# Kernel tuning notes

Hardware: AMD Instinct MI355X
Metric: run time of the kernel (lower is better)

Reference implementation:

```python
import math
import jax, jax.numpy as jnp
import numpy as np

L, H, E, D = 12, 12, 768, 64   # stack_size, mh_size, embedding_dim, dim_w_matrices
B, S = 4, 512
EPS = 1e-5


def positional_enc(seq_len, model_dim):
    # faithful: power_ind = 10000 XOR int(2*i/dim)
    i = np.arange(model_dim)
    p = np.bitwise_xor(10000, (2 * i) // model_dim).astype(np.float32)
    pos = np.arange(seq_len, dtype=np.float32)[:, None]
    ang = pos / p[None, :]
    pe = np.where(i % 2 == 0, np.sin(ang), np.cos(ang)).astype(np.float32)
    return jnp.asarray(pe)


def layer_norm(x, g, b):
    mu = jnp.mean(x, axis=-1, keepdims=True)
    var = jnp.mean(jnp.square(x - mu), axis=-1, keepdims=True)
    return (x - mu) * jax.lax.rsqrt(var + EPS) * g + b


def encoder(x, wq, wo, g1, b1, fw, fb, g2, b2):
    # x: [B,S,E]; wq: [H,E,D]; wo: [E,H*D]; fw: [E,E] (torch Linear layout)
    bs = x.shape[0] * x.shape[1]
    nb = x.reshape(bs, E)                              # flatten batch (faithful)
    q = jnp.einsum('ne,hed->hnd', nb, wq)              # q == k == v (bug kept)
    scores = jax.nn.softmax(jnp.einsum('hnd,hmd->hnm', q, q) / math.sqrt(D), axis=-1)
    z = jnp.einsum('hnm,hmd->hnd', scores, q)          # [H,BS,D]
    zc = z.reshape(H * D, bs)                          # per-head view(D,-1) + cat
    mh = (wo @ zc).reshape(x.shape)                    # [B,S,E]
    l1 = layer_norm(x + mh, g1, b1)
    ffn = l1 @ fw.T + fb
    return layer_norm(l1 + ffn, g2, b2)


def setup_inputs() -> dict:
    key = jax.random.key(0)
    ks = jax.random.split(key, 8)

    def xavier(k, shape, fan_in, fan_out):
        lim = math.sqrt(6.0 / (fan_in + fan_out))
        return jax.random.uniform(k, shape, jnp.float32, -lim, lim)

    return {
        'tokens': jax.random.normal(ks[0], (B, S, E), jnp.float32),
        'wq':    xavier(ks[1], (L, H, E, D), E, D),
        'wo':    xavier(ks[2], (L, E, H * D), E, H * D),
        'ln1_g': jnp.ones((L, E), jnp.float32),
        'ln1_b': jnp.zeros((L, E), jnp.float32),
        'ffn_w': xavier(ks[3], (L, E, E), E, E),
        'ffn_b': jnp.zeros((L, E), jnp.float32),
        'ln2_g': jnp.ones((L, E), jnp.float32),
        'ln2_b': jnp.zeros((L, E), jnp.float32),
    }


def reference(tokens, wq, wo, ln1_g, ln1_b, ffn_w, ffn_b, ln2_g, ln2_b):
    pe = positional_enc(tokens.shape[1], tokens.shape[2])
    # faithful: layer 0 applied once on pe+tokens, then ALL layers (0 again) in loop
    x = encoder(pe + tokens, wq[0], wo[0], ln1_g[0], ln1_b[0],
                ffn_w[0], ffn_b[0], ln2_g[0], ln2_b[0])
    for l in range(L):
        x = encoder(x, wq[l], wo[l], ln1_g[l], ln1_b[l],
                    ffn_w[l], ffn_b[l], ln2_g[l], ln2_b[l])
    return x
```

## Files before the change

### kernel.cpp

```cpp
#include <hip/hip_runtime.h>
#include <hip/hip_bf16.h>


#define BS_TOK 2048
#define EMB 768
#define NH 12
#define HD 64
#define WQN (12 * NH * EMB * HD)

typedef __attribute__((ext_vector_type(8))) short bf16x8;
typedef __attribute__((ext_vector_type(4))) short bf16x4;
typedef __attribute__((ext_vector_type(4))) float f32x4;

__device__ __forceinline__ short f2bf(float f) {
  union { __hip_bfloat16 h; short s; } u;
  u.h = __float2bfloat16(f);
  return u.s;
}

#define MFMA16(a, b, c) __builtin_amdgcn_mfma_f32_16x16x32_bf16(a, b, c, 0, 0, 0)
#define SW64(r, k) ((r) * 64 + ((((k) >> 3) ^ ((r) & 7)) << 3) + ((k) & 7))
#define BAR() asm volatile("s_waitcnt lgkmcnt(0)\n\ts_barrier" ::: "memory")

__global__ __launch_bounds__(256) void cvt_weights_kernel(const float* __restrict__ wo,
                                                          const float* __restrict__ fw,
                                                          short* __restrict__ wob,
                                                          short* __restrict__ fwb) {
  const float* src = blockIdx.y ? fw : wo;
  short* dst = blockIdx.y ? fwb : wob;
  int i = (blockIdx.x * 256 + threadIdx.x) * 8;
  float4 a = *(const float4*)(src + i);
  float4 b = *(const float4*)(src + i + 4);
  bf16x8 t;
  t[0] = f2bf(a.x); t[1] = f2bf(a.y); t[2] = f2bf(a.z); t[3] = f2bf(a.w);
  t[4] = f2bf(b.x); t[5] = f2bf(b.y); t[6] = f2bf(b.z); t[7] = f2bf(b.w);
  *(bf16x8*)(dst + i) = t;
}

__global__ __launch_bounds__(256) void wq_trans_kernel(const float* __restrict__ wq,
                                                       short* __restrict__ wqT) {
  __shared__ short T[64 * 64];
  const int et = blockIdx.x;
  const int lh = blockIdx.y;
  const int tid = threadIdx.x;
  const float* src = wq + ((size_t)lh * EMB + et * 64) * HD;
  {
    int r = tid >> 2, c16 = (tid & 3) << 4;
    const float* p = src + r * HD + c16;
    float4 x0 = *(const float4*)(p + 0);
    float4 x1 = *(const float4*)(p + 4);
    float4 x2 = *(const float4*)(p + 8);
    float4 x3 = *(const float4*)(p + 12);
    bf16x8 a, b;
    a[0] = f2bf(x0.x); a[1] = f2bf(x0.y); a[2] = f2bf(x0.z); a[3] = f2bf(x0.w);
    a[4] = f2bf(x1.x); a[5] = f2bf(x1.y); a[6] = f2bf(x1.z); a[7] = f2bf(x1.w);
    b[0] = f2bf(x2.x); b[1] = f2bf(x2.y); b[2] = f2bf(x2.z); b[3] = f2bf(x2.w);
    b[4] = f2bf(x3.x); b[5] = f2bf(x3.y); b[6] = f2bf(x3.z); b[7] = f2bf(x3.w);
    int g = c16 >> 3;
    *(bf16x8*)&T[r * 64 + ((g ^ (r & 7)) << 3)] = a;
    *(bf16x8*)&T[r * 64 + (((g + 1) ^ (r & 7)) << 3)] = b;
  }
  __syncthreads();
  {
    int d = tid >> 2, e16 = (tid & 3) << 4;
    bf16x8 t0, t1;
#pragma unroll
    for (int j = 0; j < 8; ++j) t0[j] = T[SW64(e16 + j, d)];
#pragma unroll
    for (int j = 0; j < 8; ++j) t1[j] = T[SW64(e16 + 8 + j, d)];
    short* q = wqT + ((size_t)lh * HD + d) * EMB + et * 64 + e16;
    *(bf16x8*)(q) = t0;
    *(bf16x8*)(q + 8) = t1;
  }
}

__global__ __launch_bounds__(256) void pe_add_kernel(const float* __restrict__ tok,
                                                     float* __restrict__ X,
                                                     short* __restrict__ Xb) {
  int idx = blockIdx.x * 256 + threadIdx.x;
  int e = idx % EMB;
  int t = idx / EMB;
  int s = t & 511;
  float p = (e < 384) ? 10000.0f : 10001.0f;
  float ang = (float)s / p;
  float pe = (e & 1) ? cosf(ang) : sinf(ang);
  float v = tok[idx] + pe;
  X[idx] = v;
  Xb[idx] = f2bf(v);
}

__device__ __forceinline__ void load64(const short* __restrict__ src, int ld,
                                       int row0, int k0, bf16x8* r, int tid) {
  int rr = tid >> 2, kb = (tid & 3) << 4;
  const short* p = src + (size_t)(row0 + rr) * ld + k0 + kb;
  r[0] = *(const bf16x8*)(p);
  r[1] = *(const bf16x8*)(p + 8);
}
__device__ __forceinline__ void write64(short* dst, const bf16x8* r, int tid) {
  int rr = tid >> 2, g = (tid & 3) << 1;
  *(bf16x8*)&dst[rr * 64 + (((g + 0) ^ (rr & 7)) << 3)] = r[0];
  *(bf16x8*)&dst[rr * 64 + (((g + 1) ^ (rr & 7)) << 3)] = r[1];
}

__device__ __forceinline__ void load128(const short* __restrict__ src, int ld,
                                        int row0, int k0, bf16x8* r, int tid) {
  int rr = tid >> 1, kb = (tid & 1) << 5;
  const short* p = src + (size_t)(row0 + rr) * ld + k0 + kb;
  r[0] = *(const bf16x8*)(p);
  r[1] = *(const bf16x8*)(p + 8);
  r[2] = *(const bf16x8*)(p + 16);
  r[3] = *(const bf16x8*)(p + 24);
}
__device__ __forceinline__ void write128(short* dst, const bf16x8* r, int tid) {
  int rr = tid >> 1, g = (tid & 1) << 2;
#pragma unroll
  for (int i = 0; i < 4; ++i)
    *(bf16x8*)&dst[rr * 64 + (((g + i) ^ (rr & 7)) << 3)] = r[i];
}

__device__ __forceinline__ void load_comb(const float* __restrict__ Op,
                                          const float* __restrict__ Lp,
                                          int k0, int col0, float4 a[4][4],
                                          float& rl, int tid) {
  const int NB = BS_TOK * EMB;
  const int NHT = NH * BS_TOK;
  int kk = tid >> 2, nb = (tid & 3) << 4;
  size_t base = (size_t)(k0 + kk) * BS_TOK + col0 + nb;
  int hq = (int)(base >> 6);
  rl = 1.0f / ((Lp[hq] + Lp[hq + NHT]) + (Lp[hq + 2 * NHT] + Lp[hq + 3 * NHT]));
#pragma unroll
  for (int z = 0; z < 4; ++z)
#pragma unroll
    for (int q4 = 0; q4 < 4; ++q4)
      a[z][q4] = *(const float4*)(Op + base + (size_t)z * NB + q4 * 4);
}
__device__ __forceinline__ void write_comb(short* dst, const float4 a[4][4],
                                           float rl, int tid) {
  int kk = tid >> 2, nb = (tid & 3) << 4;
#pragma unroll
  for (int q4 = 0; q4 < 4; ++q4) {
    dst[SW64(nb + q4 * 4 + 0, kk)] =
        f2bf(((a[0][q4].x + a[1][q4].x) + (a[2][q4].x + a[3][q4].x)) * rl);
    dst[SW64(nb + q4 * 4 + 1, kk)] =
        f2bf(((a[0][q4].y + a[1][q4].y) + (a[2][q4].y + a[3][q4].y)) * rl);
    dst[SW64(nb + q4 * 4 + 2, kk)] =
        f2bf(((a[0][q4].z + a[1][q4].z) + (a[2][q4].z + a[3][q4].z)) * rl);
    dst[SW64(nb + q4 * 4 + 3, kk)] =
        f2bf(((a[0][q4].w + a[1][q4].w) + (a[2][q4].w + a[3][q4].w)) * rl);
  }
}

#define GEMM_TILE_COMPUTE(As, Bs, acc)                                              \
  {                                                                                 \
    _Pragma("unroll") for (int s = 0; s < 2; ++s) {                                 \
      int ra = (w << 4) + l15;                                                      \
      bf16x8 af = *(const bf16x8*)&As[ra * 64 + ((((s << 2) + quad) ^ (ra & 7)) << 3)]; \
      _Pragma("unroll") for (int nt = 0; nt < 4; ++nt) {                            \
        int rb = (nt << 4) + l15;                                                   \
        bf16x8 bf = *(const bf16x8*)&Bs[rb * 64 + ((((s << 2) + quad) ^ (rb & 7)) << 3)]; \
        acc[nt] = MFMA16(af, bf, acc[nt]);                                          \
      }                                                                             \
    }                                                                               \
  }

#define GEMM_TILE_COMPUTE2(As, Bs, acc)                                             \
  {                                                                                 \
    _Pragma("unroll") for (int s = 0; s < 2; ++s) {                                 \
      bf16x8 af[2];                                                                 \
      _Pragma("unroll") for (int u = 0; u < 2; ++u) {                               \
        int ra = (w << 5) + (u << 4) + l15;                                         \
        af[u] = *(const bf16x8*)&As[ra * 64 + ((((s << 2) + quad) ^ (ra & 7)) << 3)]; \
      }                                                                             \
      _Pragma("unroll") for (int nt = 0; nt < 4; ++nt) {                            \
        int rb = (nt << 4) + l15;                                                   \
        bf16x8 bf = *(const bf16x8*)&Bs[rb * 64 + ((((s << 2) + quad) ^ (rb & 7)) << 3)]; \
        acc[0][nt] = MFMA16(af[0], bf, acc[0][nt]);                                 \
        acc[1][nt] = MFMA16(af[1], bf, acc[1][nt]);                                 \
      }                                                                             \
    }                                                                               \
  }

__global__ __launch_bounds__(256) void gemm_q_kernel(const short* __restrict__ Xb,
                                                     const short* __restrict__ WqT,
                                                     short* __restrict__ Qo,
                                                     short* __restrict__ Qt) {
  __shared__ short As[2][64 * 64];
  __shared__ short Bs[2][64 * 64];
  const int m0 = blockIdx.x * 64;
  const int h = blockIdx.y;
  const int tid = threadIdx.x;
  const int w = tid >> 6, lane = tid & 63, l15 = lane & 15, quad = lane >> 4;
  const short* wqh = WqT + (size_t)h * (HD * EMB);
  f32x4 acc[4] = {};
  bf16x8 ar[2], br[2];
  load64(Xb, EMB, m0, 0, ar, tid);
  load64(wqh, EMB, 0, 0, br, tid);
  write64(As[0], ar, tid);
  write64(Bs[0], br, tid);
  load64(Xb, EMB, m0, 64, ar, tid);
  load64(wqh, EMB, 0, 64, br, tid);
  BAR();
  for (int k0 = 0; k0 < EMB; k0 += 64) {
    const int cur = (k0 >> 6) & 1;
    const short* Ac = As[cur];
    const short* Bc = Bs[cur];
    GEMM_TILE_COMPUTE(Ac, Bc, acc);
    if (k0 + 64 < EMB) {
      write64((short*)As[cur ^ 1], ar, tid);
      write64((short*)Bs[cur ^ 1], br, tid);
      if (k0 + 128 < EMB) {
        load64(Xb, EMB, m0, k0 + 128, ar, tid);
        load64(wqh, EMB, 0, k0 + 128, br, tid);
      }
    }
    BAR();
  }
  short* T = (short*)As[0];
#pragma unroll
  for (int nt = 0; nt < 4; ++nt)
#pragma unroll
    for (int r = 0; r < 4; ++r)
      T[SW64((w << 4) + (quad << 2) + r, (nt << 4) + l15)] = f2bf(acc[nt][r]);
  __syncthreads();
  {
    int r2 = tid >> 2, kb = (tid & 3) << 4;
    int g = kb >> 3;
    bf16x8 q0v = *(const bf16x8*)&T[r2 * 64 + ((g ^ (r2 & 7)) << 3)];
    bf16x8 q1v = *(const bf16x8*)&T[r2 * 64 + (((g + 1) ^ (r2 & 7)) << 3)];
    short* qo = Qo + (size_t)h * (BS_TOK * HD) + (size_t)(m0 + r2) * HD + kb;
    *(bf16x8*)(qo) = q0v;
    *(bf16x8*)(qo + 8) = q1v;
  }
  {
    int d = tid >> 2, tok0 = (tid & 3) << 4;
    bf16x8 t0, t1;
#pragma unroll
    for (int j = 0; j < 8; ++j) t0[j] = T[SW64(tok0 + j, d)];
#pragma unroll
    for (int j = 0; j < 8; ++j) t1[j] = T[SW64(tok0 + 8 + j, d)];
    short* qt = Qt + (size_t)h * (HD * BS_TOK) + (size_t)d * BS_TOK + m0 + tok0;
    *(bf16x8*)(qt) = t0;
    *(bf16x8*)(qt + 8) = t1;
  }
}

__global__ __launch_bounds__(256, 3) void attn_mfma_kernel(const short* __restrict__ Q,
                                                           const short* __restrict__ Qt,
                                                           float* __restrict__ Opart,
                                                           float* __restrict__ Lpart) {
  __shared__ short Ks[2][64 * 64];
  __shared__ short Vt[2][64 * 64];
  __shared__ short Pw[4][32 * 64];
  const int h = blockIdx.y;
  const int q0 = blockIdx.x * 128;
  const int kt0 = blockIdx.z * 8;
  const int tid = threadIdx.x;
  const int lane = tid & 63;
  const int wv = tid >> 6;
  const int l15 = lane & 15;
  const int quad = lane >> 4;
  const short* Qh = Q + (size_t)h * (BS_TOK * HD);
  const short* Qth = Qt + (size_t)h * (HD * BS_TOK);
  short* myP = Pw[wv];

  bf16x8 qf[2][2];
#pragma unroll
  for (int sub = 0; sub < 2; ++sub) {
    const short* qp = Qh + (size_t)(q0 + wv * 32 + sub * 16 + l15) * HD + quad * 8;
    qf[sub][0] = *(const bf16x8*)(qp);
    qf[sub][1] = *(const bf16x8*)(qp + 32);
  }

  f32x4 o[2][4] = {};
  float lpl[2] = {0.f, 0.f};

  bf16x8 kreg[2], vreg[2];
#pragma unroll
  for (int i = 0; i < 2; ++i) {
    int c = i * 256 + tid;
    kreg[i] = *(const bf16x8*)(Qh + (size_t)kt0 * 4096 + c * 8);
    vreg[i] = *(const bf16x8*)(Qth + (size_t)(c >> 3) * BS_TOK + kt0 * 64 + (c & 7) * 8);
  }
#pragma unroll
  for (int i = 0; i < 2; ++i) {
    int c = i * 256 + tid, row = c >> 3, g = c & 7;
    *(bf16x8*)&Ks[0][row * 64 + ((g ^ (row & 7)) << 3)] = kreg[i];
    *(bf16x8*)&Vt[0][row * 64 + ((g ^ (row & 7)) << 3)] = vreg[i];
  }
#pragma unroll
  for (int i = 0; i < 2; ++i) {
    int c = i * 256 + tid;
    kreg[i] = *(const bf16x8*)(Qh + (size_t)(kt0 + 1) * 4096 + c * 8);
    vreg[i] = *(const bf16x8*)(Qth + (size_t)(c >> 3) * BS_TOK + (kt0 + 1) * 64 + (c & 7) * 8);
  }
  BAR();

  for (int kt = 0; kt < 8; ++kt) {
    const short* K_ = Ks[kt & 1];
    const short* V_ = Vt[kt & 1];

    f32x4 s[2][4];
    __builtin_amdgcn_s_setprio(1);
#pragma unroll
    for (int ct = 0; ct < 4; ++ct) {
      int row = ct * 16 + l15;
      bf16x8 kf0 = *(const bf16x8*)(&K_[row * 64 + ((quad ^ (row & 7)) << 3)]);
      bf16x8 kf1 = *(const bf16x8*)(&K_[row * 64 + (((4 + quad) ^ (row & 7)) << 3)]);
#pragma unroll
      for (int sub = 0; sub < 2; ++sub) {
        f32x4 a = (f32x4){0.f, 0.f, 0.f, 0.f};
        a = MFMA16(kf0, qf[sub][0], a);
        a = MFMA16(kf1, qf[sub][1], a);
        s[sub][ct] = a;
      }
    }
    __builtin_amdgcn_s_setprio(0);

#pragma unroll
    for (int sub = 0; sub < 2; ++sub) {
      int prow = sub * 16 + l15;
#pragma unroll
      for (int ct = 0; ct < 4; ++ct) {
        bf16x4 pv4;
#pragma unroll
        for (int r = 0; r < 4; ++r) {
          float p = exp2f(s[sub][ct][r] * 0.18033688011112042f);
          lpl[sub] += p;
          pv4[r] = f2bf(p);
        }
        int g = 2 * ct + (quad >> 1);
        *(bf16x4*)&myP[prow * 64 + ((g ^ (prow & 7)) << 3) + ((quad & 1) << 2)] = pv4;
      }
    }

    __builtin_amdgcn_s_setprio(1);
#pragma unroll
    for (int ks = 0; ks < 2; ++ks) {
      int c = ks * 4 + quad;
      bf16x8 pf0 = *(const bf16x8*)(&myP[l15 * 64 + ((c ^ (l15 & 7)) << 3)]);
      bf16x8 pf1 = *(const bf16x8*)(&myP[(16 + l15) * 64 + ((c ^ (l15 & 7)) << 3)]);
#pragma unroll
      for (int dt = 0; dt < 4; ++dt) {
        int row = dt * 16 + l15;
        bf16x8 vf = *(const bf16x8*)(&V_[row * 64 + ((c ^ (row & 7)) << 3)]);
        o[0][dt] = MFMA16(pf0, vf, o[0][dt]);
        o[1][dt] = MFMA16(pf1, vf, o[1][dt]);
      }
    }
    __builtin_amdgcn_s_setprio(0);

    if (kt + 1 < 8) {
      short* Kn = (short*)Ks[(kt & 1) ^ 1];
      short* Vn = (short*)Vt[(kt & 1) ^ 1];
#pragma unroll
      for (int i = 0; i < 2; ++i) {
        int c = i * 256 + tid, row = c >> 3, g = c & 7;
        *(bf16x8*)&Kn[row * 64 + ((g ^ (row & 7)) << 3)] = kreg[i];
        *(bf16x8*)&Vn[row * 64 + ((g ^ (row & 7)) << 3)] = vreg[i];
      }
      if (kt + 2 < 8) {
        int gt = kt0 + kt + 2;
#pragma unroll
        for (int i = 0; i < 2; ++i) {
          int c = i * 256 + tid;
          kreg[i] = *(const bf16x8*)(Qh + (size_t)gt * 4096 + c * 8);
          vreg[i] = *(const bf16x8*)(Qth + (size_t)(c >> 3) * BS_TOK + gt * 64 + (c & 7) * 8);
        }
      }
    }
    BAR();
  }

#pragma unroll
  for (int sub = 0; sub < 2; ++sub) {
    lpl[sub] += __shfl_xor(lpl[sub], 16, 64);
    lpl[sub] += __shfl_xor(lpl[sub], 32, 64);
  }

  const int NB = BS_TOK * EMB;
  float* Oh = Opart + (size_t)blockIdx.z * NB + (size_t)h * (BS_TOK * HD);
  float* Lh = Lpart + ((size_t)blockIdx.z * NH + h) * BS_TOK;
  if (quad == 0) {
    Lh[q0 + wv * 32 + l15] = lpl[0];
    Lh[q0 + wv * 32 + 16 + l15] = lpl[1];
  }
#pragma unroll
  for (int sub = 0; sub < 2; ++sub)
#pragma unroll
    for (int r = 0; r < 4; ++r) {
      int qrow = q0 + wv * 32 + sub * 16 + quad * 4 + r;
#pragma unroll
      for (int dt = 0; dt < 4; ++dt)
        Oh[(size_t)qrow * HD + dt * 16 + l15] = o[sub][dt][r];
    }
}

__global__ __launch_bounds__(256) void gemm_out_kernel(const short* __restrict__ Wob,
                                                       const float* __restrict__ Op,
                                                       const float* __restrict__ Lp,
                                                       float* __restrict__ Pp) {
  __shared__ short As[2][128 * 64];
  __shared__ short Bs[2][64 * 64];
  const int n0 = blockIdx.x * 64;
  const int m0 = blockIdx.y * 128;
  const int kz = blockIdx.z * 384;
  const int tid = threadIdx.x;
  const int w = tid >> 6, lane = tid & 63, l15 = lane & 15, quad = lane >> 4;
  f32x4 acc[2][4] = {};
  bf16x8 ar[4];
  float4 ca[4][4];
  float rl;
  load128(Wob, EMB, m0, kz, ar, tid);
  load_comb(Op, Lp, kz, n0, ca, rl, tid);
  write128((short*)As[0], ar, tid);
  write_comb((short*)Bs[0], ca, rl, tid);
  load128(Wob, EMB, m0, kz + 64, ar, tid);
  load_comb(Op, Lp, kz + 64, n0, ca, rl, tid);
  BAR();
  for (int k0 = 0; k0 < 384; k0 += 64) {
    const int cur = (k0 >> 6) & 1;
    const short* Ac = As[cur];
    const short* Bc = Bs[cur];
    GEMM_TILE_COMPUTE2(Ac, Bc, acc);
    if (k0 + 64 < 384) {
      write128((short*)As[cur ^ 1], ar, tid);
      write_comb((short*)Bs[cur ^ 1], ca, rl, tid);
      if (k0 + 128 < 384) {
        load128(Wob, EMB, m0, kz + k0 + 128, ar, tid);
        load_comb(Op, Lp, kz + k0 + 128, n0, ca, rl, tid);
      }
    }
    BAR();
  }
  float* P = Pp + (size_t)blockIdx.z * (BS_TOK * EMB);
#pragma unroll
  for (int u = 0; u < 2; ++u)
#pragma unroll
    for (int nt = 0; nt < 4; ++nt)
#pragma unroll
      for (int r = 0; r < 4; ++r)
        P[(size_t)(m0 + (w << 5) + (u << 4) + (quad << 2) + r) * BS_TOK + n0 +
          (nt << 4) + l15] = acc[u][nt][r];
}

__global__ __launch_bounds__(256) void gemm_ffn_kernel(const short* __restrict__ L1b,
                                                       const short* __restrict__ Fwb,
                                                       const float* __restrict__ Fb,
                                                       float* __restrict__ Pp) {
  __shared__ short As[2][128 * 64];
  __shared__ short Bs[2][64 * 64];
  const int m0 = blockIdx.x * 128;
  const int n0 = blockIdx.y * 64;
  const int kz = blockIdx.z * 384;
  const int tid = threadIdx.x;
  const int w = tid >> 6, lane = tid & 63, l15 = lane & 15, quad = lane >> 4;
  f32x4 acc[2][4] = {};
  bf16x8 ar[4], br[2];
  load128(L1b, EMB, m0, kz, ar, tid);
  load64(Fwb, EMB, n0, kz, br, tid);
  write128((short*)As[0], ar, tid);
  write64((short*)Bs[0], br, tid);
  load128(L1b, EMB, m0, kz + 64, ar, tid);
  load64(Fwb, EMB, n0, kz + 64, br, tid);
  BAR();
  for (int k0 = 0; k0 < 384; k0 += 64) {
    const int cur = (k0 >> 6) & 1;
    const short* Ac = As[cur];
    const short* Bc = Bs[cur];
    GEMM_TILE_COMPUTE2(Ac, Bc, acc);
    if (k0 + 64 < 384) {
      write128((short*)As[cur ^ 1], ar, tid);
      write64((short*)Bs[cur ^ 1], br, tid);
      if (k0 + 128 < 384) {
        load128(L1b, EMB, m0, kz + k0 + 128, ar, tid);
        load64(Fwb, EMB, n0, kz + k0 + 128, br, tid);
      }
    }
    BAR();
  }
  float* P = Pp + (size_t)blockIdx.z * (BS_TOK * EMB);
  const bool addb = (blockIdx.z == 0);
#pragma unroll
  for (int nt = 0; nt < 4; ++nt) {
    float bias = addb ? Fb[n0 + (nt << 4) + l15] : 0.0f;
#pragma unroll
    for (int u = 0; u < 2; ++u)
#pragma unroll
      for (int r = 0; r < 4; ++r)
        P[(size_t)(m0 + (w << 5) + (u << 4) + (quad << 2) + r) * EMB + n0 +
          (nt << 4) + l15] = acc[u][nt][r] + bias;
  }
}

__global__ __launch_bounds__(256) void ln_kernel(const float* __restrict__ Xa,
                                                 const float* __restrict__ P,
                                                 const float* __restrict__ g,
                                                 const float* __restrict__ bb,
                                                 float* __restrict__ Out,
                                                 short* __restrict__ Outb) {
  const int NB = BS_TOK * EMB;
  const int wv = threadIdx.x >> 6, lane = threadIdx.x & 63;
  const int t = blockIdx.x * 4 + wv;
  const float* xa = Xa + (size_t)t * EMB;
  const float* p0 = P + (size_t)t * EMB;
  const float* p1 = p0 + NB;
  float4 v[3];
  float s = 0.f;
#pragma unroll
  for (int i = 0; i < 3; ++i) {
    int e = lane * 4 + i * 256;
    float4 a = *(const float4*)(xa + e);
    float4 b = *(const float4*)(p0 + e);
    float4 c = *(const float4*)(p1 + e);
    v[i].x = a.x + b.x + c.x;
    v[i].y = a.y + b.y + c.y;
    v[i].z = a.z + b.z + c.z;
    v[i].w = a.w + b.w + c.w;
    s += v[i].x + v[i].y + v[i].z + v[i].w;
  }
#pragma unroll
  for (int o = 32; o > 0; o >>= 1) s += __shfl_xor(s, o, 64);
  float mu = s * (1.0f / EMB);
  float q = 0.f;
#pragma unroll
  for (int i = 0; i < 3; ++i) {
    float dx = v[i].x - mu, dy = v[i].y - mu, dz = v[i].z - mu, dw = v[i].w - mu;
    q += dx * dx + dy * dy + dz * dz + dw * dw;
  }
#pragma unroll
  for (int o = 32; o > 0; o >>= 1) q += __shfl_xor(q, o, 64);
  float var = q * (1.0f / EMB);
  float r = rsqrtf(var + 1e-5f);
#pragma unroll
  for (int i = 0; i < 3; ++i) {
    int e = lane * 4 + i * 256;
    float4 gg = *(const float4*)(g + e);
    float4 bv = *(const float4*)(bb + e);
    float4 res;
    res.x = (v[i].x - mu) * r * gg.x + bv.x;
    res.y = (v[i].y - mu) * r * gg.y + bv.y;
    res.z = (v[i].z - mu) * r * gg.z + bv.z;
    res.w = (v[i].w - mu) * r * gg.w + bv.w;
    *(float4*)(Out + (size_t)t * EMB + e) = res;
    bf16x4 ob;
    ob[0] = f2bf(res.x);
    ob[1] = f2bf(res.y);
    ob[2] = f2bf(res.z);
    ob[3] = f2bf(res.w);
    *(bf16x4*)(Outb + (size_t)t * EMB + e) = ob;
  }
}

extern "C" void kernel_launch(void* const* d_in, const int* in_sizes, int n_in,
                              void* d_out, int out_size, void* d_ws, size_t ws_size,
                              hipStream_t stream) {
  const float* tok = (const float*)d_in[0];
  const float* wq = (const float*)d_in[1];
  const float* wo = (const float*)d_in[2];
  const float* g1 = (const float*)d_in[3];
  const float* b1 = (const float*)d_in[4];
  const float* fw = (const float*)d_in[5];
  const float* fb = (const float*)d_in[6];
  const float* g2 = (const float*)d_in[7];
  const float* b2 = (const float*)d_in[8];
  const int NB = BS_TOK * EMB;
  float* bufA = (float*)d_ws;
  float* bufB = bufA + NB;
  float* bufC = bufB + NB;
  float* bufD = bufC + NB;
  float* opart = bufD + NB;
  short* XbA = (short*)(opart + 4 * (size_t)NB);
  short* L1b = XbA + NB;
  short* Qbf = L1b + NB;
  short* Qtb = Qbf + NB;
  short* wqTb = Qtb + NB;
  short* wob = wqTb + WQN;
  short* fwb = wob + WQN;
  float* Lpart = (float*)(fwb + WQN);

  cvt_weights_kernel<<<dim3(WQN / (256 * 8), 2), 256, 0, stream>>>(wo, fw, wob, fwb);
  wq_trans_kernel<<<dim3(12, 12 * NH), 256, 0, stream>>>(wq, wqTb);
  pe_add_kernel<<<NB / 256, 256, 0, stream>>>(tok, bufA, XbA);
  for (int it = 0; it < 13; ++it) {
    int l = (it == 0) ? 0 : it - 1;
    gemm_q_kernel<<<dim3(32, NH), 256, 0, stream>>>(
        XbA, wqTb + (size_t)l * (NH * HD * EMB), Qbf, Qtb);
    attn_mfma_kernel<<<dim3(16, NH, 4), 256, 0, stream>>>(Qbf, Qtb, opart, Lpart);
    gemm_out_kernel<<<dim3(32, 6, 2), 256, 0, stream>>>(
        wob + (size_t)l * (EMB * EMB), opart, Lpart, bufB);
    ln_kernel<<<BS_TOK / 4, 256, 0, stream>>>(bufA, bufB, g1 + l * EMB, b1 + l * EMB,
                                              bufD, L1b);
    gemm_ffn_kernel<<<dim3(16, 12, 2), 256, 0, stream>>>(
        L1b, fwb + (size_t)l * (EMB * EMB), fb + l * EMB, bufB);
    float* ln2_dst = (it == 12) ? (float*)d_out : bufA;
    ln_kernel<<<BS_TOK / 4, 256, 0, stream>>>(bufD, bufB, g2 + l * EMB, b2 + l * EMB,
                                              ln2_dst, XbA);
  }
}
```

Measured before the change: 1.161 ms.

## Drop split-K attention partials; normalize in attention and emit bf16 Z directly

The attention kernel no longer splits the key dimension into four partial blocks that write fp32 O and row-sum partials. Each block now processes all 32 key tiles for 64 queries, normalizes by the row sum, and writes a bf16 Z tile through shared memory. The out-projection GEMM then reads bf16 Z directly instead of combining four fp32 partials, which removes a large amount of global traffic and reduction work. The trade-off is a smaller grid with longer per-block serial loops (384 blocks instead of 768) and half the queries per wave, so each loaded K/V tile is reused less.

```diff
diff --git a/kernel.cpp b/kernel.cpp
--- a/kernel.cpp
+++ b/kernel.cpp
@@ -118,36 +118,19 @@
     *(bf16x8*)&dst[rr * 64 + (((g + i) ^ (rr & 7)) << 3)] = r[i];
 }
 
-__device__ __forceinline__ void load_comb(const float* __restrict__ Op,
-                                          const float* __restrict__ Lp,
-                                          int k0, int col0, float4 a[4][4],
-                                          float& rl, int tid) {
-  const int NB = BS_TOK * EMB;
-  const int NHT = NH * BS_TOK;
+__device__ __forceinline__ void load_zc(const short* __restrict__ Zcb,
+                                        int k0, int col0, bf16x8 cr[2], int tid) {
   int kk = tid >> 2, nb = (tid & 3) << 4;
-  size_t base = (size_t)(k0 + kk) * BS_TOK + col0 + nb;
-  int hq = (int)(base >> 6);
-  rl = 1.0f / ((Lp[hq] + Lp[hq + NHT]) + (Lp[hq + 2 * NHT] + Lp[hq + 3 * NHT]));
-#pragma unroll
-  for (int z = 0; z < 4; ++z)
-#pragma unroll
-    for (int q4 = 0; q4 < 4; ++q4)
-      a[z][q4] = *(const float4*)(Op + base + (size_t)z * NB + q4 * 4);
-}
-__device__ __forceinline__ void write_comb(short* dst, const float4 a[4][4],
-                                           float rl, int tid) {
+  const short* p = Zcb + (size_t)(k0 + kk) * BS_TOK + col0 + nb;
+  cr[0] = *(const bf16x8*)(p);
+  cr[1] = *(const bf16x8*)(p + 8);
+}
+__device__ __forceinline__ void write_zc(short* dst, const bf16x8 cr[2], int tid) {
   int kk = tid >> 2, nb = (tid & 3) << 4;
 #pragma unroll
-  for (int q4 = 0; q4 < 4; ++q4) {
-    dst[SW64(nb + q4 * 4 + 0, kk)] =
-        f2bf(((a[0][q4].x + a[1][q4].x) + (a[2][q4].x + a[3][q4].x)) * rl);
-    dst[SW64(nb + q4 * 4 + 1, kk)] =
-        f2bf(((a[0][q4].y + a[1][q4].y) + (a[2][q4].y + a[3][q4].y)) * rl);
-    dst[SW64(nb + q4 * 4 + 2, kk)] =
-        f2bf(((a[0][q4].z + a[1][q4].z) + (a[2][q4].z + a[3][q4].z)) * rl);
-    dst[SW64(nb + q4 * 4 + 3, kk)] =
-        f2bf(((a[0][q4].w + a[1][q4].w) + (a[2][q4].w + a[3][q4].w)) * rl);
-  }
+  for (int j = 0; j < 8; ++j) dst[SW64(nb + j, kk)] = cr[0][j];
+#pragma unroll
+  for (int j = 0; j < 8; ++j) dst[SW64(nb + 8 + j, kk)] = cr[1][j];
 }
 
 #define GEMM_TILE_COMPUTE(As, Bs, acc)                                              \
@@ -244,16 +227,14 @@
   }
 }
 
-__global__ __launch_bounds__(256, 3) void attn_mfma_kernel(const short* __restrict__ Q,
-                                                           const short* __restrict__ Qt,
-                                                           float* __restrict__ Opart,
-                                                           float* __restrict__ Lpart) {
+__global__ __launch_bounds__(256) void attn_mfma_kernel(const short* __restrict__ Q,
+                                                        const short* __restrict__ Qt,
+                                                        short* __restrict__ Zcb) {
   __shared__ short Ks[2][64 * 64];
   __shared__ short Vt[2][64 * 64];
-  __shared__ short Pw[4][32 * 64];
+  __shared__ short Pw[4][16 * 64];
   const int h = blockIdx.y;
-  const int q0 = blockIdx.x * 128;
-  const int kt0 = blockIdx.z * 8;
+  const int q0 = blockIdx.x * 64;
   const int tid = threadIdx.x;
   const int lane = tid & 63;
   const int wv = tid >> 6;
@@ -263,23 +244,22 @@
   const short* Qth = Qt + (size_t)h * (HD * BS_TOK);
   short* myP = Pw[wv];
 
-  bf16x8 qf[2][2];
-#pragma unroll
-  for (int sub = 0; sub < 2; ++sub) {
-    const short* qp = Qh + (size_t)(q0 + wv * 32 + sub * 16 + l15) * HD + quad * 8;
-    qf[sub][0] = *(const bf16x8*)(qp);
-    qf[sub][1] = *(const bf16x8*)(qp + 32);
-  }
-
-  f32x4 o[2][4] = {};
-  float lpl[2] = {0.f, 0.f};
+  bf16x8 qf[2];
+  {
+    const short* qp = Qh + (size_t)(q0 + wv * 16 + l15) * HD + quad * 8;
+    qf[0] = *(const bf16x8*)(qp);
+    qf[1] = *(const bf16x8*)(qp + 32);
+  }
+
+  f32x4 o[4] = {};
+  float lpl = 0.f;
 
   bf16x8 kreg[2], vreg[2];
 #pragma unroll
   for (int i = 0; i < 2; ++i) {
     int c = i * 256 + tid;
-    kreg[i] = *(const bf16x8*)(Qh + (size_t)kt0 * 4096 + c * 8);
-    vreg[i] = *(const bf16x8*)(Qth + (size_t)(c >> 3) * BS_TOK + kt0 * 64 + (c & 7) * 8);
+    kreg[i] = *(const bf16x8*)(Qh + c * 8);
+    vreg[i] = *(const bf16x8*)(Qth + (size_t)(c >> 3) * BS_TOK + (c & 7) * 8);
   }
 #pragma unroll
   for (int i = 0; i < 2; ++i) {
@@ -290,66 +270,59 @@
 #pragma unroll
   for (int i = 0; i < 2; ++i) {
     int c = i * 256 + tid;
-    kreg[i] = *(const bf16x8*)(Qh + (size_t)(kt0 + 1) * 4096 + c * 8);
-    vreg[i] = *(const bf16x8*)(Qth + (size_t)(c >> 3) * BS_TOK + (kt0 + 1) * 64 + (c & 7) * 8);
+    kreg[i] = *(const bf16x8*)(Qh + 4096 + c * 8);
+    vreg[i] = *(const bf16x8*)(Qth + (size_t)(c >> 3) * BS_TOK + 64 + (c & 7) * 8);
   }
   BAR();
 
-  for (int kt = 0; kt < 8; ++kt) {
+  for (int kt = 0; kt < 32; ++kt) {
     const short* K_ = Ks[kt & 1];
     const short* V_ = Vt[kt & 1];
 
-    f32x4 s[2][4];
+    f32x4 s[4];
     __builtin_amdgcn_s_setprio(1);
 #pragma unroll
     for (int ct = 0; ct < 4; ++ct) {
-      int row = ct * 16 + l15;
-      bf16x8 kf0 = *(const bf16x8*)(&K_[row * 64 + ((quad ^ (row & 7)) << 3)]);
-      bf16x8 kf1 = *(const bf16x8*)(&K_[row * 64 + (((4 + quad) ^ (row & 7)) << 3)]);
-#pragma unroll
-      for (int sub = 0; sub < 2; ++sub) {
-        f32x4 a = (f32x4){0.f, 0.f, 0.f, 0.f};
-        a = MFMA16(kf0, qf[sub][0], a);
-        a = MFMA16(kf1, qf[sub][1], a);
-        s[sub][ct] = a;
-      }
+      f32x4 a = (f32x4){0.f, 0.f, 0.f, 0.f};
+#pragma unroll
+      for (int ks = 0; ks < 2; ++ks) {
+        int row = ct * 16 + l15;
+        int c = ks * 4 + quad;
+        bf16x8 kf = *(const bf16x8*)(&K_[row * 64 + ((c ^ (row & 7)) << 3)]);
+        a = MFMA16(kf, qf[ks], a);
+      }
+      s[ct] = a;
     }
     __builtin_amdgcn_s_setprio(0);
 
 #pragma unroll
-    for (int sub = 0; sub < 2; ++sub) {
-      int prow = sub * 16 + l15;
-#pragma unroll
-      for (int ct = 0; ct < 4; ++ct) {
-        bf16x4 pv4;
-#pragma unroll
-        for (int r = 0; r < 4; ++r) {
-          float p = exp2f(s[sub][ct][r] * 0.18033688011112042f);
-          lpl[sub] += p;
-          pv4[r] = f2bf(p);
-        }
-        int g = 2 * ct + (quad >> 1);
-        *(bf16x4*)&myP[prow * 64 + ((g ^ (prow & 7)) << 3) + ((quad & 1) << 2)] = pv4;
-      }
+    for (int ct = 0; ct < 4; ++ct) {
+      bf16x4 pv4;
+#pragma unroll
+      for (int r = 0; r < 4; ++r) {
+        float p = exp2f(s[ct][r] * 0.18033688011112042f);
+        lpl += p;
+        pv4[r] = f2bf(p);
+      }
+      int g = 2 * ct + (quad >> 1);
+      *(bf16x4*)&myP[l15 * 64 + ((g ^ (l15 & 7)) << 3) + ((quad & 1) << 2)] = pv4;
     }
 
     __builtin_amdgcn_s_setprio(1);
 #pragma unroll
     for (int ks = 0; ks < 2; ++ks) {
       int c = ks * 4 + quad;
-      bf16x8 pf0 = *(const bf16x8*)(&myP[l15 * 64 + ((c ^ (l15 & 7)) << 3)]);
-      bf16x8 pf1 = *(const bf16x8*)(&myP[(16 + l15) * 64 + ((c ^ (l15 & 7)) << 3)]);
+      bf16x8 pf = *(const bf16x8*)(&myP[l15 * 64 + ((c ^ (l15 & 7)) << 3)]);
 #pragma unroll
       for (int dt = 0; dt < 4; ++dt) {
         int row = dt * 16 + l15;
         bf16x8 vf = *(const bf16x8*)(&V_[row * 64 + ((c ^ (row & 7)) << 3)]);
-        o[0][dt] = MFMA16(pf0, vf, o[0][dt]);
-        o[1][dt] = MFMA16(pf1, vf, o[1][dt]);
+        o[dt] = MFMA16(pf, vf, o[dt]);
       }
     }
     __builtin_amdgcn_s_setprio(0);
 
-    if (kt + 1 < 8) {
+    if (kt + 1 < 32) {
       short* Kn = (short*)Ks[(kt & 1) ^ 1];
       short* Vn = (short*)Vt[(kt & 1) ^ 1];
 #pragma unroll
@@ -358,8 +331,8 @@
         *(bf16x8*)&Kn[row * 64 + ((g ^ (row & 7)) << 3)] = kreg[i];
         *(bf16x8*)&Vn[row * 64 + ((g ^ (row & 7)) << 3)] = vreg[i];
       }
-      if (kt + 2 < 8) {
-        int gt = kt0 + kt + 2;
+      if (kt + 2 < 32) {
+        int gt = kt + 2;
 #pragma unroll
         for (int i = 0; i < 2; ++i) {
           int c = i * 256 + tid;
@@ -371,33 +344,34 @@
     BAR();
   }
 
-#pragma unroll
-  for (int sub = 0; sub < 2; ++sub) {
-    lpl[sub] += __shfl_xor(lpl[sub], 16, 64);
-    lpl[sub] += __shfl_xor(lpl[sub], 32, 64);
-  }
-
-  const int NB = BS_TOK * EMB;
-  float* Oh = Opart + (size_t)blockIdx.z * NB + (size_t)h * (BS_TOK * HD);
-  float* Lh = Lpart + ((size_t)blockIdx.z * NH + h) * BS_TOK;
-  if (quad == 0) {
-    Lh[q0 + wv * 32 + l15] = lpl[0];
-    Lh[q0 + wv * 32 + 16 + l15] = lpl[1];
-  }
-#pragma unroll
-  for (int sub = 0; sub < 2; ++sub)
-#pragma unroll
-    for (int r = 0; r < 4; ++r) {
-      int qrow = q0 + wv * 32 + sub * 16 + quad * 4 + r;
-#pragma unroll
-      for (int dt = 0; dt < 4; ++dt)
-        Oh[(size_t)qrow * HD + dt * 16 + l15] = o[sub][dt][r];
-    }
+  lpl += __shfl_xor(lpl, 16, 64);
+  lpl += __shfl_xor(lpl, 32, 64);
+
+  float rl[4];
+#pragma unroll
+  for (int r = 0; r < 4; ++r)
+    rl[r] = 1.0f / __shfl(lpl, quad * 4 + r, 64);
+
+  short* T = (short*)Ks[0];
+#pragma unroll
+  for (int dt = 0; dt < 4; ++dt)
+#pragma unroll
+    for (int r = 0; r < 4; ++r)
+      T[SW64(wv * 16 + quad * 4 + r, dt * 16 + l15)] = f2bf(o[dt][r] * rl[r]);
+  __syncthreads();
+  {
+    short* zo = Zcb + (size_t)h * (BS_TOK * HD) + (size_t)q0 * HD;
+    int r2 = tid >> 2, kb = (tid & 3) << 4;
+    int g = kb >> 3;
+    bf16x8 z0 = *(const bf16x8*)&T[r2 * 64 + ((g ^ (r2 & 7)) << 3)];
+    bf16x8 z1 = *(const bf16x8*)&T[r2 * 64 + (((g + 1) ^ (r2 & 7)) << 3)];
+    *(bf16x8*)(zo + r2 * 64 + kb) = z0;
+    *(bf16x8*)(zo + r2 * 64 + kb + 8) = z1;
+  }
 }
 
 __global__ __launch_bounds__(256) void gemm_out_kernel(const short* __restrict__ Wob,
-                                                       const float* __restrict__ Op,
-                                                       const float* __restrict__ Lp,
+                                                       const short* __restrict__ Zcb,
                                                        float* __restrict__ Pp) {
   __shared__ short As[2][128 * 64];
   __shared__ short Bs[2][64 * 64];
@@ -407,15 +381,13 @@
   const int tid = threadIdx.x;
   const int w = tid >> 6, lane = tid & 63, l15 = lane & 15, quad = lane >> 4;
   f32x4 acc[2][4] = {};
-  bf16x8 ar[4];
-  float4 ca[4][4];
-  float rl;
+  bf16x8 ar[4], cr[2];
   load128(Wob, EMB, m0, kz, ar, tid);
-  load_comb(Op, Lp, kz, n0, ca, rl, tid);
+  load_zc(Zcb, kz, n0, cr, tid);
   write128((short*)As[0], ar, tid);
-  write_comb((short*)Bs[0], ca, rl, tid);
+  write_zc((short*)Bs[0], cr, tid);
   load128(Wob, EMB, m0, kz + 64, ar, tid);
-  load_comb(Op, Lp, kz + 64, n0, ca, rl, tid);
+  load_zc(Zcb, kz + 64, n0, cr, tid);
   BAR();
   for (int k0 = 0; k0 < 384; k0 += 64) {
     const int cur = (k0 >> 6) & 1;
@@ -424,10 +396,10 @@
     GEMM_TILE_COMPUTE2(Ac, Bc, acc);
     if (k0 + 64 < 384) {
       write128((short*)As[cur ^ 1], ar, tid);
-      write_comb((short*)Bs[cur ^ 1], ca, rl, tid);
+      write_zc((short*)Bs[cur ^ 1], cr, tid);
       if (k0 + 128 < 384) {
         load128(Wob, EMB, m0, kz + k0 + 128, ar, tid);
-        load_comb(Op, Lp, kz + k0 + 128, n0, ca, rl, tid);
+        load_zc(Zcb, kz + k0 + 128, n0, cr, tid);
       }
     }
     BAR();
@@ -568,15 +540,14 @@
   float* bufB = bufA + NB;
   float* bufC = bufB + NB;
   float* bufD = bufC + NB;
-  float* opart = bufD + NB;
-  short* XbA = (short*)(opart + 4 * (size_t)NB);
+  short* XbA = (short*)(bufD + NB);
   short* L1b = XbA + NB;
   short* Qbf = L1b + NB;
   short* Qtb = Qbf + NB;
-  short* wqTb = Qtb + NB;
+  short* Zcb = Qtb + NB;
+  short* wqTb = Zcb + NB;
   short* wob = wqTb + WQN;
   short* fwb = wob + WQN;
-  float* Lpart = (float*)(fwb + WQN);
 
   cvt_weights_kernel<<<dim3(WQN / (256 * 8), 2), 256, 0, stream>>>(wo, fw, wob, fwb);
   wq_trans_kernel<<<dim3(12, 12 * NH), 256, 0, stream>>>(wq, wqTb);
@@ -585,9 +556,9 @@
     int l = (it == 0) ? 0 : it - 1;
     gemm_q_kernel<<<dim3(32, NH), 256, 0, stream>>>(
         XbA, wqTb + (size_t)l * (NH * HD * EMB), Qbf, Qtb);
-    attn_mfma_kernel<<<dim3(16, NH, 4), 256, 0, stream>>>(Qbf, Qtb, opart, Lpart);
+    attn_mfma_kernel<<<dim3(32, NH), 256, 0, stream>>>(Qbf, Qtb, Zcb);
     gemm_out_kernel<<<dim3(32, 6, 2), 256, 0, stream>>>(
-        wob + (size_t)l * (EMB * EMB), opart, Lpart, bufB);
+        wob + (size_t)l * (EMB * EMB), Zcb, bufB);
     ln_kernel<<<BS_TOK / 4, 256, 0, stream>>>(bufA, bufB, g1 + l * EMB, b1 + l * EMB,
                                               bufD, L1b);
     gemm_ffn_kernel<<<dim3(16, 12, 2), 256, 0, stream>>>(
```

After: 1.199 ms. 1.03x slower.
